# Kernel optimization log

Hardware: AMD Instinct MI355X
Metric: run time of the kernel (lower is better)

## Reference

```python
import jax, jax.numpy as jnp
import numpy as np
from jax import lax

EPS = 1e-6
MATCH_THRESHOLD = 0.3
N_DISCRETE_STEPS = 5
DT = 0.01
TWO_PI = 2.0 * np.pi


def setup_inputs() -> dict:
    key = jax.random.key(0)
    ks = jax.random.split(key, 6)
    N, M, D, H, n_osc = 8192, 8192, 4, 64, 28
    detections_t = jax.random.normal(ks[0], (N, D), dtype=jnp.float32)
    detections_t1 = jax.random.normal(ks[1], (M, D), dtype=jnp.float32)
    phase_W1 = jax.random.normal(ks[2], (D, H), dtype=jnp.float32) * (1.0 / np.sqrt(D))
    phase_b1 = jax.random.normal(ks[3], (H,), dtype=jnp.float32) * 0.05
    phase_W2 = jax.random.normal(ks[4], (H, n_osc), dtype=jnp.float32) * (1.0 / np.sqrt(H))
    phase_b2 = jax.random.normal(ks[5], (n_osc,), dtype=jnp.float32) * 0.05
    # fixed oscillator frequencies buffer: [2]*4 + [6]*8 + [40]*16
    frequencies = jnp.concatenate([
        jnp.full((4,), 2.0, jnp.float32),
        jnp.full((8,), 6.0, jnp.float32),
        jnp.full((16,), 40.0, jnp.float32),
    ])
    return {
        'detections_t': detections_t,
        'detections_t1': detections_t1,
        'phase_W1': phase_W1,
        'phase_b1': phase_b1,
        'phase_W2': phase_W2,
        'phase_b2': phase_b2,
        'frequencies': frequencies,
    }


def _encode_phase(x, W1, b1, W2, b2):
    h = jax.nn.relu(x @ W1 + b1)
    raw = h @ W2 + b2
    return raw % TWO_PI  # [N, n_osc]


def _similarity(phase_a, phase_b):
    # real(sum_k e^{i a_k} e^{-i b_k}) = cos(a)@cos(b).T + sin(a)@sin(b).T
    ca, sa = jnp.cos(phase_a), jnp.sin(phase_a)
    cb, sb = jnp.cos(phase_b), jnp.sin(phase_b)
    na = jnp.sqrt(jnp.sum(ca * ca + sa * sa, axis=-1, keepdims=True)) + EPS  # [N,1]
    nb = jnp.sqrt(jnp.sum(cb * cb + sb * sb, axis=-1, keepdims=True)) + EPS  # [M,1]
    sim = (ca @ cb.T + sa @ sb.T) / (na * nb.T)  # [N, M]
    return sim


def reference(detections_t, detections_t1, phase_W1, phase_b1, phase_W2, phase_b2, frequencies):
    phase_t = _encode_phase(detections_t, phase_W1, phase_b1, phase_W2, phase_b2)
    phase_t1 = _encode_phase(detections_t1, phase_W1, phase_b1, phase_W2, phase_b2)

    # uncoupled phase advance (n_discrete_steps fixed small loop)
    phase = phase_t
    for _ in range(N_DISCRETE_STEPS):
        phase = (phase + TWO_PI * frequencies * DT) % TWO_PI

    sim = _similarity(phase, phase_t1)  # [N, M]

    N = detections_t.shape[0]
    M = detections_t1.shape[0]
    max_sims = jnp.max(sim, axis=1)
    max_idxs = jnp.argmax(sim, axis=1)
    order = jnp.argsort(-max_sims)  # descending

    def body(i, carry):
        matches, used = carry
        idx = order[i]
        j = max_idxs[idx]
        ok = jnp.logical_and(jnp.logical_not(used[j]), max_sims[idx] > MATCH_THRESHOLD)
        matches = matches.at[idx].set(jnp.where(ok, j, -1))
        used = used.at[j].set(jnp.logical_or(used[j], ok))
        return (matches, used)

    matches0 = jnp.full((N,), -1, dtype=jnp.int32)
    used0 = jnp.zeros((M,), dtype=bool)
    matches, _ = lax.fori_loop(0, N, body, (matches0, used0))
    return (matches, sim)
```

## Files before the change

kernel.cpp:

```cpp
#include <hip/hip_runtime.h>
#include <math.h>

#define NR 8192
#define N_OSC 28
#define TWO_PI_F 6.28318530717958647692f
#define PLANE 524288

typedef __attribute__((ext_vector_type(8))) short s16x8;
typedef __attribute__((ext_vector_type(16))) float f32x16;
typedef __attribute__((ext_vector_type(4))) float f32x4;
typedef __attribute__((ext_vector_type(4))) unsigned int u32x4;

#define AS3(p) ((__attribute__((address_space(3))) void*)(p))
#define AS1C(p) ((const __attribute__((address_space(1))) void*)(p))

__device__ __forceinline__ float modpos(float x) {
    float r = fmodf(x, TWO_PI_F);
    if (r < 0.0f) r += TWO_PI_F;
    return r;
}
__device__ __forceinline__ unsigned fmono(float f) {
    unsigned u = __float_as_uint(f);
    return (u & 0x80000000u) ? ~u : (u | 0x80000000u);
}
__device__ __forceinline__ unsigned short f2bf(float f) {
    unsigned u = __float_as_uint(f);
    return (unsigned short)((u + 0x7FFFu + ((u >> 16) & 1u)) >> 16);
}
__device__ __forceinline__ float bf2f(unsigned short h) {
    return __uint_as_float(((unsigned)h) << 16);
}


__global__ __launch_bounds__(256, 1) void encode_kernel(
    const float* __restrict__ detA, const float* __restrict__ detB,
    const float* __restrict__ W1, const float* __restrict__ b1,
    const float* __restrict__ W2, const float* __restrict__ b2,
    const float* __restrict__ freq,
    unsigned short* __restrict__ tabA, unsigned short* __restrict__ tabB)
{
    __shared__ float sW1[4 * 64];
    __shared__ float sb1[64];
    __shared__ float sW2[64 * N_OSC];
    __shared__ float sb2[N_OSC];
    __shared__ float sDelta[N_OSC];

    int t = threadIdx.x;
    for (int i = t; i < 4 * 64; i += 256) sW1[i] = W1[i];
    for (int i = t; i < 64; i += 256) sb1[i] = b1[i];
    for (int i = t; i < 64 * N_OSC; i += 256) sW2[i] = W2[i];
    for (int i = t; i < N_OSC; i += 256) {
        sb2[i] = b2[i];
        sDelta[i] = (TWO_PI_F * freq[i]) * 0.01f;
    }
    __syncthreads();

    int gid = blockIdx.x * 256 + t;
    bool isA = gid < NR;
    int row = isA ? gid : gid - NR;
    const float* det = isA ? detA : detB;
    unsigned short* tab = isA ? tabA : tabB;

    float4 xv = *(const float4*)(det + (size_t)row * 4);
    float x0 = xv.x, x1 = xv.y, x2 = xv.z, x3 = xv.w;

    float h[64];
#pragma unroll
    for (int j = 0; j < 64; ++j) {
        float a = x0 * sW1[0 * 64 + j];
        a += x1 * sW1[1 * 64 + j];
        a += x2 * sW1[2 * 64 + j];
        a += x3 * sW1[3 * 64 + j];
        a += sb1[j];
        h[j] = fmaxf(a, 0.0f);
    }

    float raw[N_OSC];
#pragma unroll
    for (int o = 0; o < N_OSC; ++o) raw[o] = 0.0f;
#pragma unroll
    for (int j = 0; j < 64; ++j) {
        float hj = h[j];
#pragma unroll
        for (int o = 0; o < N_OSC; ++o) raw[o] += hj * sW2[j * N_OSC + o];
    }

    float cv[N_OSC], sv[N_OSC];
    float csum = 0.0f;
#pragma unroll
    for (int o = 0; o < N_OSC; ++o) {
        float p = raw[o] + sb2[o];
        p = modpos(p);
        if (isA) {
            float d = sDelta[o];
#pragma unroll
            for (int s = 0; s < 5; ++s) { p = modpos(p + d); }
        }
        float sn, cs;
        sincosf(p, &sn, &cs);
        cv[o] = cs; sv[o] = sn;
        csum += cs * cs + sn * sn;
    }
    float irn = 1.0f / (sqrtf(csum) + 1e-6f);

    unsigned h2[32], m2[32], l2[32];
#pragma unroll
    for (int i = 0; i < 32; ++i) { h2[i] = 0u; m2[i] = 0u; l2[i] = 0u; }

#pragma unroll
    for (int o = 0; o < N_OSC; ++o) {
        {
            float x = cv[o] * irn;
            unsigned short v0 = f2bf(x); float r1 = x - bf2f(v0);
            unsigned short v1 = f2bf(r1); float r2 = r1 - bf2f(v1);
            unsigned short v2 = f2bf(r2);
            const int k = o, i = k >> 1, sh = (k & 1) * 16;
            h2[i] |= ((unsigned)v0) << sh;
            m2[i] |= ((unsigned)v1) << sh;
            l2[i] |= ((unsigned)v2) << sh;
        }
        {
            float x = sv[o] * irn;
            unsigned short v0 = f2bf(x); float r1 = x - bf2f(v0);
            unsigned short v1 = f2bf(r1); float r2 = r1 - bf2f(v1);
            unsigned short v2 = f2bf(r2);
            const int k = 28 + o, i = k >> 1, sh = (k & 1) * 16;
            h2[i] |= ((unsigned)v0) << sh;
            m2[i] |= ((unsigned)v1) << sh;
            l2[i] |= ((unsigned)v2) << sh;
        }
    }

    size_t gbase = (size_t)(row >> 5) * 2048 + (size_t)(row & 31) * 8;
#pragma unroll
    for (int c = 0; c < 8; ++c) {
        size_t off = gbase + (size_t)(c >> 1) * 512 + (size_t)(c & 1) * 256;
        u32x4 vh, vm, vl;
#pragma unroll
        for (int e = 0; e < 4; ++e) {
            vh[e] = h2[c * 4 + e]; vm[e] = m2[c * 4 + e]; vl[e] = l2[c * 4 + e];
        }
        *(u32x4*)(tab + off) = vh;
        *(u32x4*)(tab + PLANE + off) = vm;
        *(u32x4*)(tab + 2 * PLANE + off) = vl;
    }
}

#define MFMA(a, b, c) __builtin_amdgcn_mfma_f32_32x32x16_bf16((a), (b), (c), 0, 0, 0)

__global__ __launch_bounds__(128, 1) void sim_kernel(
    const unsigned short* __restrict__ tabA, const unsigned short* __restrict__ tabB,
    float* __restrict__ simOut, unsigned long long* __restrict__ rowMax)
{
    __shared__ __align__(16) unsigned char smem[33280];
    unsigned short* Ash = (unsigned short*)smem;

    int bid = blockIdx.x;
    int swz = (bid & 7) * 1024 + (bid >> 3);
    int bx = swz & 63, by = swz >> 6;
    int r0 = by * 64, c0 = bx * 128;

    int t = threadIdx.x, w = t >> 6, l = t & 63;
    int wc = w;
    int l31 = l & 31, h5 = l >> 5;
    int gB = (c0 + wc * 64) >> 5;
    int gr0 = r0 >> 5;
    size_t l8 = (size_t)l * 8;

#define GLD(tab, pl, g, ks) \
    (*(const s16x8*)((tab) + (size_t)(pl) * PLANE + (size_t)(g) * 2048 + (size_t)(ks) * 512 + l8))

    s16x8 bh0[4], bh1[4], bm0[4], bm1[4], bl0[4], bl1[4];
#pragma unroll
    for (int ks = 0; ks < 4; ++ks) {
        bh0[ks] = GLD(tabB, 0, gB, ks);  bh1[ks] = GLD(tabB, 0, gB + 1, ks);
        bm0[ks] = GLD(tabB, 1, gB, ks);  bm1[ks] = GLD(tabB, 1, gB + 1, ks);
        bl0[ks] = GLD(tabB, 2, gB, ks);  bl1[ks] = GLD(tabB, 2, gB + 1, ks);
    }
#undef GLD

#pragma unroll
    for (int i = 0; i < 12; ++i) {
        int unit = w * 12 + i;
        int p = unit >> 3, rem = unit & 7;
        int g = rem >> 2, ks = rem & 3;
        const unsigned short* src = tabA + (size_t)p * PLANE
            + (size_t)(gr0 + g) * 2048 + (size_t)ks * 512 + l8;
        __builtin_amdgcn_global_load_lds(AS1C(src), AS3(Ash + unit * 512), 16, 0, 0);
    }
    __builtin_amdgcn_sched_barrier(0);
    __syncthreads();

    f32x16 acc00, acc01, acc10, acc11;
#pragma unroll
    for (int r = 0; r < 16; ++r) { acc00[r] = 0.f; acc01[r] = 0.f; acc10[r] = 0.f; acc11[r] = 0.f; }

    const char* Ab = (const char*)Ash + (size_t)l * 16;
#define LDA(p, g, ks) (*(const s16x8*)(Ab + (((p) * 8 + (g) * 4 + (ks)) * 1024)))

#pragma unroll
    for (int ks = 0; ks < 4; ++ks) {
        s16x8 ah0 = LDA(0, 0, ks), ah1 = LDA(0, 1, ks);
        s16x8 am0 = LDA(1, 0, ks), am1 = LDA(1, 1, ks);
        s16x8 al0 = LDA(2, 0, ks), al1 = LDA(2, 1, ks);

        acc00 = MFMA(bh0[ks], ah0, acc00); acc01 = MFMA(bh1[ks], ah0, acc01);
        acc10 = MFMA(bh0[ks], ah1, acc10); acc11 = MFMA(bh1[ks], ah1, acc11);
        acc00 = MFMA(bm0[ks], ah0, acc00); acc01 = MFMA(bm1[ks], ah0, acc01);
        acc10 = MFMA(bm0[ks], ah1, acc10); acc11 = MFMA(bm1[ks], ah1, acc11);
        acc00 = MFMA(bh0[ks], am0, acc00); acc01 = MFMA(bh1[ks], am0, acc01);
        acc10 = MFMA(bh0[ks], am1, acc10); acc11 = MFMA(bh1[ks], am1, acc11);
        acc00 = MFMA(bm0[ks], am0, acc00); acc01 = MFMA(bm1[ks], am0, acc01);
        acc10 = MFMA(bm0[ks], am1, acc10); acc11 = MFMA(bm1[ks], am1, acc11);
        acc00 = MFMA(bl0[ks], ah0, acc00); acc01 = MFMA(bl1[ks], ah0, acc01);
        acc10 = MFMA(bl0[ks], ah1, acc10); acc11 = MFMA(bl1[ks], ah1, acc11);
        acc00 = MFMA(bh0[ks], al0, acc00); acc01 = MFMA(bh1[ks], al0, acc01);
        acc10 = MFMA(bh0[ks], al1, acc10); acc11 = MFMA(bh1[ks], al1, acc11);
    }
#undef LDA

    int cbase = c0 + wc * 64 + 4 * h5;
    unsigned long long key0 = 0ull, key1 = 0ull;
#pragma unroll
    for (int r = 0; r < 16; ++r) {
        int pa = (r & 3) + 8 * (r >> 2);
        unsigned col0 = (unsigned)(cbase + pa);
        unsigned col1 = (unsigned)(cbase + 32 + pa);
        unsigned long long k;
        k = ((unsigned long long)fmono(acc00[r]) << 32) | (unsigned long long)(0xFFFFFFFFu - col0);
        if (k > key0) key0 = k;
        k = ((unsigned long long)fmono(acc01[r]) << 32) | (unsigned long long)(0xFFFFFFFFu - col1);
        if (k > key0) key0 = k;
        k = ((unsigned long long)fmono(acc10[r]) << 32) | (unsigned long long)(0xFFFFFFFFu - col0);
        if (k > key1) key1 = k;
        k = ((unsigned long long)fmono(acc11[r]) << 32) | (unsigned long long)(0xFFFFFFFFu - col1);
        if (k > key1) key1 = k;
    }
    {
        unsigned lo = (unsigned)key0, hi = (unsigned)(key0 >> 32);
        unsigned olo = __shfl_xor(lo, 32, 64), ohi = __shfl_xor(hi, 32, 64);
        unsigned long long o = ((unsigned long long)ohi << 32) | olo;
        if (o > key0) key0 = o;
        lo = (unsigned)key1; hi = (unsigned)(key1 >> 32);
        olo = __shfl_xor(lo, 32, 64); ohi = __shfl_xor(hi, 32, 64);
        o = ((unsigned long long)ohi << 32) | olo;
        if (o > key1) key1 = o;
    }
    if (l < 32) {
        atomicMax(&rowMax[r0 + l], key0);
        atomicMax(&rowMax[r0 + 32 + l], key1);
    }

    __syncthreads();
    float* scr = (float*)(smem + w * 16640);

#pragma unroll
    for (int r = 0; r < 16; ++r) {
        int pa = (r & 3) + 8 * (r >> 2) + 4 * h5;
        scr[l31 * 65 + pa]             = acc00[r];
        scr[l31 * 65 + 32 + pa]        = acc01[r];
        scr[(32 + l31) * 65 + pa]      = acc10[r];
        scr[(32 + l31) * 65 + 32 + pa] = acc11[r];
    }

#pragma unroll
    for (int s = 0; s < 16; ++s) {
        int lr = 4 * s + (l >> 4);
        f32x4 v = *(const f32x4*)&scr[lr * 65 + (l & 15) * 4];
        __builtin_nontemporal_store(v,
            (f32x4*)&simOut[(size_t)(r0 + lr) * NR + c0 + wc * 64 + (l & 15) * 4]);
    }
}

__global__ __launch_bounds__(256) void rowwin_kernel(
    const unsigned long long* __restrict__ rowMax,
    unsigned long long* __restrict__ colWin,
    float* __restrict__ outMatches)
{
    int r = blockIdx.x * 256 + threadIdx.x;
    if (r >= NR) return;
    outMatches[r] = -1.0f;
    unsigned long long key = rowMax[r];
    unsigned m = (unsigned)(key >> 32);
    unsigned bits = (m & 0x80000000u) ? (m ^ 0x80000000u) : ~m;
    float ms = __uint_as_float(bits);
    unsigned col = 0xFFFFFFFFu - (unsigned)key;
    if (ms > 0.3f) {
        unsigned long long ck = ((unsigned long long)m << 32)
                              | (unsigned long long)(0xFFFFFFFFu - (unsigned)r);
        atomicMax(&colWin[col], ck);
    }
}

__global__ __launch_bounds__(256) void colfin_kernel(
    const unsigned long long* __restrict__ colWin,
    float* __restrict__ outMatches)
{
    int j = blockIdx.x * 256 + threadIdx.x;
    if (j >= NR) return;
    unsigned long long w = colWin[j];
    if (w != 0ull) {
        unsigned r = 0xFFFFFFFFu - (unsigned)w;
        outMatches[r] = (float)j;
    }
}

extern "C" void kernel_launch(void* const* d_in, const int* in_sizes, int n_in,
                              void* d_out, int out_size, void* d_ws, size_t ws_size,
                              hipStream_t stream) {
    const float* detA = (const float*)d_in[0];
    const float* detB = (const float*)d_in[1];
    const float* W1   = (const float*)d_in[2];
    const float* b1   = (const float*)d_in[3];
    const float* W2   = (const float*)d_in[4];
    const float* b2   = (const float*)d_in[5];
    const float* freq = (const float*)d_in[6];
    float* out = (float*)d_out;

    char* ws = (char*)d_ws;
    unsigned short* tabA = (unsigned short*)(ws);
    unsigned short* tabB = (unsigned short*)(ws + 3145728);
    unsigned long long* rowMax = (unsigned long long*)(ws + 6291456);
    unsigned long long* colWin = (unsigned long long*)(ws + 6356992);

    (void)hipMemsetAsync(rowMax, 0, NR * 8, stream);
    (void)hipMemsetAsync(colWin, 0, NR * 8, stream);

    encode_kernel<<<64, 256, 0, stream>>>(detA, detB, W1, b1, W2, b2, freq,
                                          tabA, tabB);
    sim_kernel<<<8192, 128, 0, stream>>>(tabA, tabB, out + NR, rowMax);
    rowwin_kernel<<<NR / 256, 256, 0, stream>>>(rowMax, colWin, out);
    colfin_kernel<<<NR / 256, 256, 0, stream>>>(colWin, out);
}
```

Measured before the change: 142.1 us.

## Enlarge sim tile to 128x128 with staged A planes and fold memsets into encode

The sim kernel now uses 256-thread blocks covering a 128x128 output tile. All three B planes and the A planes are staged through LDS, and the A mid and low planes are loaded into a reused buffer between MFMA phases. This halves the grid, raises data reuse per block and frees the per-lane B registers. The two rowMax/colWin memsets are dropped; encode_kernel zeroes those buffers instead, and it now runs as 128 blocks of 128 threads. The costs are more barriers, a larger LDS footprint per block (80KB) and possibly lower occupancy.

Measured after the change: 161.0 us. 1.13x slower.

```diff
diff --git a/kernel.cpp b/kernel.cpp
--- a/kernel.cpp
+++ b/kernel.cpp
@@ -32,12 +32,13 @@
 }
 
 
-__global__ __launch_bounds__(256, 1) void encode_kernel(
+__global__ __launch_bounds__(128) void encode_kernel(
     const float* __restrict__ detA, const float* __restrict__ detB,
     const float* __restrict__ W1, const float* __restrict__ b1,
     const float* __restrict__ W2, const float* __restrict__ b2,
     const float* __restrict__ freq,
-    unsigned short* __restrict__ tabA, unsigned short* __restrict__ tabB)
+    unsigned short* __restrict__ tabA, unsigned short* __restrict__ tabB,
+    unsigned long long* __restrict__ rowMax, unsigned long long* __restrict__ colWin)
 {
     __shared__ float sW1[4 * 64];
     __shared__ float sb1[64];
@@ -46,20 +47,22 @@
     __shared__ float sDelta[N_OSC];
 
     int t = threadIdx.x;
-    for (int i = t; i < 4 * 64; i += 256) sW1[i] = W1[i];
-    for (int i = t; i < 64; i += 256) sb1[i] = b1[i];
-    for (int i = t; i < 64 * N_OSC; i += 256) sW2[i] = W2[i];
-    for (int i = t; i < N_OSC; i += 256) {
+    for (int i = t; i < 4 * 64; i += 128) sW1[i] = W1[i];
+    for (int i = t; i < 64; i += 128) sb1[i] = b1[i];
+    for (int i = t; i < 64 * N_OSC; i += 128) sW2[i] = W2[i];
+    for (int i = t; i < N_OSC; i += 128) {
         sb2[i] = b2[i];
         sDelta[i] = (TWO_PI_F * freq[i]) * 0.01f;
     }
     __syncthreads();
 
-    int gid = blockIdx.x * 256 + t;
+    int gid = blockIdx.x * 128 + t;
     bool isA = gid < NR;
     int row = isA ? gid : gid - NR;
     const float* det = isA ? detA : detB;
     unsigned short* tab = isA ? tabA : tabB;
+
+    if (isA) rowMax[gid] = 0ull; else colWin[gid - NR] = 0ull;
 
     float4 xv = *(const float4*)(det + (size_t)row * 4);
     float x0 = xv.x, x1 = xv.y, x2 = xv.z, x3 = xv.w;
@@ -148,76 +151,106 @@
 
 #define MFMA(a, b, c) __builtin_amdgcn_mfma_f32_32x32x16_bf16((a), (b), (c), 0, 0, 0)
 
-__global__ __launch_bounds__(128, 1) void sim_kernel(
+__global__ __launch_bounds__(256) void sim_kernel(
     const unsigned short* __restrict__ tabA, const unsigned short* __restrict__ tabB,
     float* __restrict__ simOut, unsigned long long* __restrict__ rowMax)
 {
-    __shared__ __align__(16) unsigned char smem[33280];
-    unsigned short* Ash = (unsigned short*)smem;
+    __shared__ __align__(16) unsigned char smem[81920];
 
     int bid = blockIdx.x;
-    int swz = (bid & 7) * 1024 + (bid >> 3);
+    int swz = (bid & 7) * 512 + (bid >> 3);
     int bx = swz & 63, by = swz >> 6;
-    int r0 = by * 64, c0 = bx * 128;
+    int r0 = by * 128, c0 = bx * 128;
 
     int t = threadIdx.x, w = t >> 6, l = t & 63;
-    int wc = w;
+    int wr = w >> 1, wc = w & 1;
     int l31 = l & 31, h5 = l >> 5;
-    int gB = (c0 + wc * 64) >> 5;
-    int gr0 = r0 >> 5;
+    int gA0 = r0 >> 5, gB0 = c0 >> 5;
     size_t l8 = (size_t)l * 8;
-
-#define GLD(tab, pl, g, ks) \
-    (*(const s16x8*)((tab) + (size_t)(pl) * PLANE + (size_t)(g) * 2048 + (size_t)(ks) * 512 + l8))
-
-    s16x8 bh0[4], bh1[4], bm0[4], bm1[4], bl0[4], bl1[4];
-#pragma unroll
-    for (int ks = 0; ks < 4; ++ks) {
-        bh0[ks] = GLD(tabB, 0, gB, ks);  bh1[ks] = GLD(tabB, 0, gB + 1, ks);
-        bm0[ks] = GLD(tabB, 1, gB, ks);  bm1[ks] = GLD(tabB, 1, gB + 1, ks);
-        bl0[ks] = GLD(tabB, 2, gB, ks);  bl1[ks] = GLD(tabB, 2, gB + 1, ks);
-    }
-#undef GLD
 
 #pragma unroll
     for (int i = 0; i < 12; ++i) {
         int unit = w * 12 + i;
-        int p = unit >> 3, rem = unit & 7;
+        int p = unit >> 4, rem = unit & 15;
         int g = rem >> 2, ks = rem & 3;
-        const unsigned short* src = tabA + (size_t)p * PLANE
-            + (size_t)(gr0 + g) * 2048 + (size_t)ks * 512 + l8;
-        __builtin_amdgcn_global_load_lds(AS1C(src), AS3(Ash + unit * 512), 16, 0, 0);
+        const unsigned short* src = tabB + (size_t)p * PLANE
+            + (size_t)(gB0 + g) * 2048 + (size_t)ks * 512 + l8;
+        __builtin_amdgcn_global_load_lds(AS1C(src), AS3(smem + unit * 1024), 16, 0, 0);
+    }
+#pragma unroll
+    for (int i = 0; i < 4; ++i) {
+        int unit = w * 4 + i;
+        int g = unit >> 2, ks = unit & 3;
+        const unsigned short* src = tabA
+            + (size_t)(gA0 + g) * 2048 + (size_t)ks * 512 + l8;
+        __builtin_amdgcn_global_load_lds(AS1C(src), AS3(smem + 49152 + unit * 1024), 16, 0, 0);
     }
     __builtin_amdgcn_sched_barrier(0);
     __syncthreads();
 
+#pragma unroll
+    for (int i = 0; i < 4; ++i) {
+        int unit = w * 4 + i;
+        int g = unit >> 2, ks = unit & 3;
+        const unsigned short* src = tabA + PLANE
+            + (size_t)(gA0 + g) * 2048 + (size_t)ks * 512 + l8;
+        __builtin_amdgcn_global_load_lds(AS1C(src), AS3(smem + 65536 + unit * 1024), 16, 0, 0);
+    }
+    __builtin_amdgcn_sched_barrier(0);
+
     f32x16 acc00, acc01, acc10, acc11;
 #pragma unroll
     for (int r = 0; r < 16; ++r) { acc00[r] = 0.f; acc01[r] = 0.f; acc10[r] = 0.f; acc11[r] = 0.f; }
 
-    const char* Ab = (const char*)Ash + (size_t)l * 16;
-#define LDA(p, g, ks) (*(const s16x8*)(Ab + (((p) * 8 + (g) * 4 + (ks)) * 1024)))
+#define LDB(p, gg, ks) (*(const s16x8*)(smem + (((p) * 16 + (2 * wc + (gg)) * 4 + (ks)) * 1024) + (size_t)l * 16))
+#define LDA(buf, gg, ks) (*(const s16x8*)(smem + 49152 + (buf) * 16384 + (((2 * wr + (gg)) * 4 + (ks)) * 1024) + (size_t)l * 16))
+
+    s16x8 bh0[4], bh1[4];
 
 #pragma unroll
     for (int ks = 0; ks < 4; ++ks) {
         s16x8 ah0 = LDA(0, 0, ks), ah1 = LDA(0, 1, ks);
-        s16x8 am0 = LDA(1, 0, ks), am1 = LDA(1, 1, ks);
-        s16x8 al0 = LDA(2, 0, ks), al1 = LDA(2, 1, ks);
-
+        bh0[ks] = LDB(0, 0, ks); bh1[ks] = LDB(0, 1, ks);
+        s16x8 q0 = LDB(1, 0, ks), q1 = LDB(1, 1, ks);
+        s16x8 p0 = LDB(2, 0, ks), p1 = LDB(2, 1, ks);
         acc00 = MFMA(bh0[ks], ah0, acc00); acc01 = MFMA(bh1[ks], ah0, acc01);
         acc10 = MFMA(bh0[ks], ah1, acc10); acc11 = MFMA(bh1[ks], ah1, acc11);
-        acc00 = MFMA(bm0[ks], ah0, acc00); acc01 = MFMA(bm1[ks], ah0, acc01);
-        acc10 = MFMA(bm0[ks], ah1, acc10); acc11 = MFMA(bm1[ks], ah1, acc11);
+        acc00 = MFMA(q0, ah0, acc00); acc01 = MFMA(q1, ah0, acc01);
+        acc10 = MFMA(q0, ah1, acc10); acc11 = MFMA(q1, ah1, acc11);
+        acc00 = MFMA(p0, ah0, acc00); acc01 = MFMA(p1, ah0, acc01);
+        acc10 = MFMA(p0, ah1, acc10); acc11 = MFMA(p1, ah1, acc11);
+    }
+    __syncthreads();
+
+#pragma unroll
+    for (int i = 0; i < 4; ++i) {
+        int unit = w * 4 + i;
+        int g = unit >> 2, ks = unit & 3;
+        const unsigned short* src = tabA + 2 * PLANE
+            + (size_t)(gA0 + g) * 2048 + (size_t)ks * 512 + l8;
+        __builtin_amdgcn_global_load_lds(AS1C(src), AS3(smem + 49152 + unit * 1024), 16, 0, 0);
+    }
+    __builtin_amdgcn_sched_barrier(0);
+
+#pragma unroll
+    for (int ks = 0; ks < 4; ++ks) {
+        s16x8 am0 = LDA(1, 0, ks), am1 = LDA(1, 1, ks);
+        s16x8 q0 = LDB(1, 0, ks), q1 = LDB(1, 1, ks);
         acc00 = MFMA(bh0[ks], am0, acc00); acc01 = MFMA(bh1[ks], am0, acc01);
         acc10 = MFMA(bh0[ks], am1, acc10); acc11 = MFMA(bh1[ks], am1, acc11);
-        acc00 = MFMA(bm0[ks], am0, acc00); acc01 = MFMA(bm1[ks], am0, acc01);
-        acc10 = MFMA(bm0[ks], am1, acc10); acc11 = MFMA(bm1[ks], am1, acc11);
-        acc00 = MFMA(bl0[ks], ah0, acc00); acc01 = MFMA(bl1[ks], ah0, acc01);
-        acc10 = MFMA(bl0[ks], ah1, acc10); acc11 = MFMA(bl1[ks], ah1, acc11);
+        acc00 = MFMA(q0, am0, acc00); acc01 = MFMA(q1, am0, acc01);
+        acc10 = MFMA(q0, am1, acc10); acc11 = MFMA(q1, am1, acc11);
+    }
+    __syncthreads();
+
+#pragma unroll
+    for (int ks = 0; ks < 4; ++ks) {
+        s16x8 al0 = LDA(0, 0, ks), al1 = LDA(0, 1, ks);
         acc00 = MFMA(bh0[ks], al0, acc00); acc01 = MFMA(bh1[ks], al0, acc01);
         acc10 = MFMA(bh0[ks], al1, acc10); acc11 = MFMA(bh1[ks], al1, acc11);
     }
 #undef LDA
+#undef LDB
 
     int cbase = c0 + wc * 64 + 4 * h5;
     unsigned long long key0 = 0ull, key1 = 0ull;
@@ -247,20 +280,31 @@
         if (o > key1) key1 = o;
     }
     if (l < 32) {
-        atomicMax(&rowMax[r0 + l], key0);
-        atomicMax(&rowMax[r0 + 32 + l], key1);
+        atomicMax(&rowMax[r0 + wr * 64 + l], key0);
+        atomicMax(&rowMax[r0 + wr * 64 + 32 + l], key1);
     }
 
     __syncthreads();
     float* scr = (float*)(smem + w * 16640);
 
 #pragma unroll
-    for (int r = 0; r < 16; ++r) {
-        int pa = (r & 3) + 8 * (r >> 2) + 4 * h5;
-        scr[l31 * 65 + pa]             = acc00[r];
-        scr[l31 * 65 + 32 + pa]        = acc01[r];
-        scr[(32 + l31) * 65 + pa]      = acc10[r];
-        scr[(32 + l31) * 65 + 32 + pa] = acc11[r];
+    for (int ag = 0; ag < 2; ++ag) {
+#pragma unroll
+        for (int bg = 0; bg < 2; ++bg) {
+#pragma unroll
+            for (int k = 0; k < 4; ++k) {
+                f32x4 v;
+#pragma unroll
+                for (int e = 0; e < 4; ++e) {
+                    float x = ag == 0 ? (bg == 0 ? acc00[4 * k + e] : acc01[4 * k + e])
+                                      : (bg == 0 ? acc10[4 * k + e] : acc11[4 * k + e]);
+                    v[e] = x;
+                }
+                int rrow = ag * 32 + l31;
+                int ccol = bg * 32 + 8 * k + 4 * h5;
+                *(f32x4*)&scr[rrow * 65 + ccol] = v;
+            }
+        }
     }
 
 #pragma unroll
@@ -268,7 +312,7 @@
         int lr = 4 * s + (l >> 4);
         f32x4 v = *(const f32x4*)&scr[lr * 65 + (l & 15) * 4];
         __builtin_nontemporal_store(v,
-            (f32x4*)&simOut[(size_t)(r0 + lr) * NR + c0 + wc * 64 + (l & 15) * 4]);
+            (f32x4*)&simOut[(size_t)(r0 + wr * 64 + lr) * NR + c0 + wc * 64 + (l & 15) * 4]);
     }
 }
 
@@ -323,12 +367,9 @@
     unsigned long long* rowMax = (unsigned long long*)(ws + 6291456);
     unsigned long long* colWin = (unsigned long long*)(ws + 6356992);
 
-    (void)hipMemsetAsync(rowMax, 0, NR * 8, stream);
-    (void)hipMemsetAsync(colWin, 0, NR * 8, stream);
-
-    encode_kernel<<<64, 256, 0, stream>>>(detA, detB, W1, b1, W2, b2, freq,
-                                          tabA, tabB);
-    sim_kernel<<<8192, 128, 0, stream>>>(tabA, tabB, out + NR, rowMax);
+    encode_kernel<<<128, 128, 0, stream>>>(detA, detB, W1, b1, W2, b2, freq,
+                                           tabA, tabB, rowMax, colWin);
+    sim_kernel<<<4096, 256, 0, stream>>>(tabA, tabB, out + NR, rowMax);
     rowwin_kernel<<<NR / 256, 256, 0, stream>>>(rowMax, colWin, out);
     colfin_kernel<<<NR / 256, 256, 0, stream>>>(colWin, out);
 }
```
